# Kernel tuning notes

Measured on AMD Instinct MI355X. Metric: run time of the kernel, lower is better.

## Reference

```python
import jax, jax.numpy as jnp
import numpy as np

# Module config (matches init_kwargs)
STRIDE = (2, 2)
PAD = (1, 1)
OUT_PAD = (1, 1)
K = (3, 3)
MULTIPLIER = 2.0
CIN, COUT = 256, 256


def setup_inputs() -> dict:
    key = jax.random.key(0)
    k1, k2, k3 = jax.random.split(key, 3)
    B, H_in, W_in = 32, 64, 64
    x = jax.random.normal(k1, (B, CIN, H_in, W_in), dtype=jnp.float32)
    # kaiming-uniform-ish scale for weight, small uniform bias
    fan_in = CIN * K[0] * K[1]
    bound = 1.0 / np.sqrt(fan_in)
    weight = jax.random.uniform(k2, (CIN, COUT, K[0], K[1]), dtype=jnp.float32,
                                minval=-bound, maxval=bound)
    bias = jax.random.uniform(k3, (COUT,), dtype=jnp.float32, minval=-bound, maxval=bound)
    return {"x": x, "weight": weight, "bias": bias}


def _valid_mask(n_in, k, stride, pad, n_out):
    # mask[i, t] = 1.0 if 0 <= i*stride - pad + t < n_out
    i = jnp.arange(n_in)[:, None]
    t = jnp.arange(k)[None, :]
    o = i * stride - pad + t
    return ((o >= 0) & (o < n_out)).astype(jnp.float32)


def reference(x, weight, bias):
    B, Cin, H_in, W_in = x.shape
    Kh, Kw = weight.shape[2], weight.shape[3]
    H_out = (H_in - 1) * STRIDE[0] - 2 * PAD[0] + (Kh - 1) + OUT_PAD[0] + 1
    W_out = (W_in - 1) * STRIDE[1] - 2 * PAD[1] + (Kw - 1) + OUT_PAD[1] + 1

    mh = _valid_mask(H_in, Kh, STRIDE[0], PAD[0], H_out)  # [H_in, Kh]
    mw = _valid_mask(W_in, Kw, STRIDE[1], PAD[1], W_out)  # [W_in, Kw]

    # Stage 1: U[b,c,kh,kw] = sum_{h,w} x[b,c,h,w] * mh[h,kh] * mw[w,kw]
    U = jnp.einsum('bchw,hk,wl->bckl', x, mh, mw)
    # Stage 2: spatial sum per output channel
    S = jnp.einsum('bckl,cokl->bo', U, weight)
    spatial = H_out * W_out
    out = MULTIPLIER * (S / spatial + bias[None, :])
    return out.reshape(B, weight.shape[1], 1, 1)
```

## Files before the change

### kernel.cpp

```cpp
#include <hip/hip_runtime.h>

#define CIN   256
#define COUT  256
#define NB    32
#define HIN   64
#define WIN   64
#define SPATIAL_OUT 16384.0f
#define MULT  2.0f

__global__ __launch_bounds__(256) void reduce_x_kernel(
    const float* __restrict__ x, float* __restrict__ xs)
{
    const int bc = blockIdx.x;
    const float4* p = (const float4*)(x + (size_t)bc * (HIN * WIN));
    const int t = threadIdx.x;

    float s_all = 0.f, s_r0 = 0.f, s_c0 = 0.f, x00 = 0.f;
#pragma unroll
    for (int i = 0; i < 4; ++i) {
        const int idx = t + 256 * i;
        const float4 v = p[idx];
        s_all += v.x + v.y + v.z + v.w;
        if (idx < 16)        s_r0 += v.x + v.y + v.z + v.w;
        if ((idx & 15) == 0) s_c0 += v.x;
        if (idx == 0)        x00 = v.x;
    }

#pragma unroll
    for (int off = 32; off > 0; off >>= 1) {
        s_all += __shfl_down(s_all, off);
        s_r0  += __shfl_down(s_r0,  off);
        s_c0  += __shfl_down(s_c0,  off);
    }

    __shared__ float red[4][3];
    const int wave = t >> 6, lane = t & 63;
    if (lane == 0) { red[wave][0] = s_all; red[wave][1] = s_r0; red[wave][2] = s_c0; }
    __syncthreads();
    if (t == 0) {
        float a = 0.f, r = 0.f, c = 0.f;
#pragma unroll
        for (int w = 0; w < 4; ++w) { a += red[w][0]; r += red[w][1]; c += red[w][2]; }
        float4 o; o.x = a; o.y = r; o.z = c; o.w = x00;
        ((float4*)xs)[bc] = o;
    }
}

__global__ __launch_bounds__(256) void reduce_w_kernel(
    const float* __restrict__ w, float* __restrict__ ws)
{
    const int co = blockIdx.x * 256 + threadIdx.x;
    const float* p = w + (size_t)co * 9;
    const float w0 = p[0], w1 = p[1], w2 = p[2],
                w3 = p[3], w4 = p[4], w5 = p[5],
                w6 = p[6], w7 = p[7], w8 = p[8];
    const float wsum = w0 + w1 + w2 + w3 + w4 + w5 + w6 + w7 + w8;
    const float wr   = w0 + w1 + w2;
    const float wc   = w0 + w3 + w6;
    const int c = co >> 8, o = co & 255;
    ws[(c * 4 + 0) * 256 + o] = wsum;
    ws[(c * 4 + 1) * 256 + o] = wr;
    ws[(c * 4 + 2) * 256 + o] = wc;
    ws[(c * 4 + 3) * 256 + o] = w0;
}

__global__ __launch_bounds__(256) void finalize_kernel(
    const float* __restrict__ xs, const float* __restrict__ ws,
    const float* __restrict__ bias, float* __restrict__ out)
{
    const int b = blockIdx.x, o = threadIdx.x;
    __shared__ float4 sx[CIN];
    sx[o] = ((const float4*)xs)[b * CIN + o];
    __syncthreads();

    float acc = 0.f;
#pragma unroll 4
    for (int c = 0; c < CIN; ++c) {
        const float4 s = sx[c];
        const float wsum = ws[(c * 4 + 0) * 256 + o];
        const float wr   = ws[(c * 4 + 1) * 256 + o];
        const float wc   = ws[(c * 4 + 2) * 256 + o];
        const float w00  = ws[(c * 4 + 3) * 256 + o];
        acc += s.x * wsum - s.y * wr - s.z * wc + s.w * w00;
    }
    out[b * 256 + o] = MULT * (acc * (1.0f / SPATIAL_OUT) + bias[o]);
}

extern "C" void kernel_launch(void* const* d_in, const int* in_sizes, int n_in,
                              void* d_out, int out_size, void* d_ws, size_t ws_size,
                              hipStream_t stream)
{
    const float* x      = (const float*)d_in[0];
    const float* weight = (const float*)d_in[1];
    const float* bias   = (const float*)d_in[2];
    float* out = (float*)d_out;

    float* xs = (float*)d_ws;
    float* ws = xs + (size_t)NB * CIN * 4;

    reduce_x_kernel<<<NB * CIN, 256, 0, stream>>>(x, xs);
    reduce_w_kernel<<<CIN, 256, 0, stream>>>(weight, ws);
    finalize_kernel<<<NB, 256, 0, stream>>>(xs, ws, bias, out);
}
```

Measured before the change: 217.0 us.

## Merge x and weight stat kernels, pack weight stats as float4, split finalize

```diff
diff --git a/kernel.cpp b/kernel.cpp
--- a/kernel.cpp
+++ b/kernel.cpp
@@ -5,85 +5,89 @@
 #define NB    32
 #define HIN   64
 #define WIN   64
-#define SPATIAL_OUT 16384.0f
+#define INV_SPATIAL (1.0f / 16384.0f)
 #define MULT  2.0f
 
-__global__ __launch_bounds__(256) void reduce_x_kernel(
-    const float* __restrict__ x, float* __restrict__ xs)
+__global__ __launch_bounds__(256) void stats_kernel(
+    const float* __restrict__ x, const float* __restrict__ w,
+    float4* __restrict__ xs, float4* __restrict__ ws4)
 {
-    const int bc = blockIdx.x;
-    const float4* p = (const float4*)(x + (size_t)bc * (HIN * WIN));
-    const int t = threadIdx.x;
+    const int blk = blockIdx.x;
+    const int t   = threadIdx.x;
 
-    float s_all = 0.f, s_r0 = 0.f, s_c0 = 0.f, x00 = 0.f;
+    if (blk < NB * CIN) {
+        const float4* p = (const float4*)(x + (size_t)blk * (HIN * WIN));
+        float s_all = 0.f, s_r0 = 0.f, s_c0 = 0.f, x00 = 0.f;
 #pragma unroll
-    for (int i = 0; i < 4; ++i) {
-        const int idx = t + 256 * i;
-        const float4 v = p[idx];
-        s_all += v.x + v.y + v.z + v.w;
-        if (idx < 16)        s_r0 += v.x + v.y + v.z + v.w;
-        if ((idx & 15) == 0) s_c0 += v.x;
-        if (idx == 0)        x00 = v.x;
-    }
-
+        for (int i = 0; i < 4; ++i) {
+            const int idx = t + 256 * i;
+            const float4 v = p[idx];
+            s_all += v.x + v.y + v.z + v.w;
+            if (idx < 16)        s_r0 += v.x + v.y + v.z + v.w;
+            if ((idx & 15) == 0) s_c0 += v.x;
+            if (idx == 0)        x00 = v.x;
+        }
 #pragma unroll
-    for (int off = 32; off > 0; off >>= 1) {
-        s_all += __shfl_down(s_all, off);
-        s_r0  += __shfl_down(s_r0,  off);
-        s_c0  += __shfl_down(s_c0,  off);
-    }
-
-    __shared__ float red[4][3];
-    const int wave = t >> 6, lane = t & 63;
-    if (lane == 0) { red[wave][0] = s_all; red[wave][1] = s_r0; red[wave][2] = s_c0; }
-    __syncthreads();
-    if (t == 0) {
-        float a = 0.f, r = 0.f, c = 0.f;
+        for (int off = 32; off > 0; off >>= 1) {
+            s_all += __shfl_down(s_all, off);
+            s_r0  += __shfl_down(s_r0,  off);
+            s_c0  += __shfl_down(s_c0,  off);
+        }
+        __shared__ float red[4][3];
+        const int wave = t >> 6, lane = t & 63;
+        if (lane == 0) { red[wave][0] = s_all; red[wave][1] = s_r0; red[wave][2] = s_c0; }
+        __syncthreads();
+        if (t == 0) {
+            float a = 0.f, r = 0.f, c = 0.f;
 #pragma unroll
-        for (int w = 0; w < 4; ++w) { a += red[w][0]; r += red[w][1]; c += red[w][2]; }
-        float4 o; o.x = a; o.y = r; o.z = c; o.w = x00;
-        ((float4*)xs)[bc] = o;
+            for (int wv = 0; wv < 4; ++wv) { a += red[wv][0]; r += red[wv][1]; c += red[wv][2]; }
+            float4 o4; o4.x = a; o4.y = r; o4.z = c; o4.w = x00;
+            xs[blk] = o4;
+        }
+    } else {
+        const int c = blk - NB * CIN;
+        const float* p = w + ((size_t)c * COUT + t) * 9;
+        const float w0 = p[0], w1 = p[1], w2 = p[2],
+                    w3 = p[3], w4 = p[4], w5 = p[5],
+                    w6 = p[6], w7 = p[7], w8 = p[8];
+        float4 o4;
+        o4.x = w0 + w1 + w2 + w3 + w4 + w5 + w6 + w7 + w8;
+        o4.y = w0 + w1 + w2;
+        o4.z = w0 + w3 + w6;
+        o4.w = w0;
+        ws4[c * COUT + t] = o4;
     }
 }
 
-__global__ __launch_bounds__(256) void reduce_w_kernel(
-    const float* __restrict__ w, float* __restrict__ ws)
-{
-    const int co = blockIdx.x * 256 + threadIdx.x;
-    const float* p = w + (size_t)co * 9;
-    const float w0 = p[0], w1 = p[1], w2 = p[2],
-                w3 = p[3], w4 = p[4], w5 = p[5],
-                w6 = p[6], w7 = p[7], w8 = p[8];
-    const float wsum = w0 + w1 + w2 + w3 + w4 + w5 + w6 + w7 + w8;
-    const float wr   = w0 + w1 + w2;
-    const float wc   = w0 + w3 + w6;
-    const int c = co >> 8, o = co & 255;
-    ws[(c * 4 + 0) * 256 + o] = wsum;
-    ws[(c * 4 + 1) * 256 + o] = wr;
-    ws[(c * 4 + 2) * 256 + o] = wc;
-    ws[(c * 4 + 3) * 256 + o] = w0;
-}
-
-__global__ __launch_bounds__(256) void finalize_kernel(
-    const float* __restrict__ xs, const float* __restrict__ ws,
+__global__ __launch_bounds__(1024) void finalize_kernel(
+    const float4* __restrict__ xs, const float4* __restrict__ ws4,
     const float* __restrict__ bias, float* __restrict__ out)
 {
-    const int b = blockIdx.x, o = threadIdx.x;
+    const int b   = blockIdx.x;
+    const int t   = threadIdx.x;
+    const int o   = t & 255;
+    const int seg = t >> 8;
+
     __shared__ float4 sx[CIN];
-    sx[o] = ((const float4*)xs)[b * CIN + o];
+    __shared__ float  part[4][COUT];
+    if (t < CIN) sx[t] = xs[b * CIN + t];
     __syncthreads();
 
     float acc = 0.f;
-#pragma unroll 4
-    for (int c = 0; c < CIN; ++c) {
-        const float4 s = sx[c];
-        const float wsum = ws[(c * 4 + 0) * 256 + o];
-        const float wr   = ws[(c * 4 + 1) * 256 + o];
-        const float wc   = ws[(c * 4 + 2) * 256 + o];
-        const float w00  = ws[(c * 4 + 3) * 256 + o];
-        acc += s.x * wsum - s.y * wr - s.z * wc + s.w * w00;
+    const int c0 = seg * 64;
+#pragma unroll 8
+    for (int i = 0; i < 64; ++i) {
+        const int c = c0 + i;
+        const float4 s  = sx[c];
+        const float4 wv = ws4[c * COUT + o];
+        acc += s.x * wv.x - s.y * wv.y - s.z * wv.z + s.w * wv.w;
     }
-    out[b * 256 + o] = MULT * (acc * (1.0f / SPATIAL_OUT) + bias[o]);
+    part[seg][o] = acc;
+    __syncthreads();
+    if (t < COUT) {
+        const float a = part[0][t] + part[1][t] + part[2][t] + part[3][t];
+        out[b * COUT + t] = MULT * (a * INV_SPATIAL + bias[t]);
+    }
 }
 
 extern "C" void kernel_launch(void* const* d_in, const int* in_sizes, int n_in,
@@ -95,10 +99,9 @@
     const float* bias   = (const float*)d_in[2];
     float* out = (float*)d_out;
 
-    float* xs = (float*)d_ws;
-    float* ws = xs + (size_t)NB * CIN * 4;
+    float4* xs  = (float4*)d_ws;
+    float4* ws4 = xs + (size_t)NB * CIN;
 
-    reduce_x_kernel<<<NB * CIN, 256, 0, stream>>>(x, xs);
-    reduce_w_kernel<<<CIN, 256, 0, stream>>>(weight, ws);
-    finalize_kernel<<<NB, 256, 0, stream>>>(xs, ws, bias, out);
+    stats_kernel<<<NB * CIN + CIN, 256, 0, stream>>>(x, weight, xs, ws4);
+    finalize_kernel<<<NB, 1024, 0, stream>>>(xs, ws4, bias, out);
 }
```

New measurement: 200.8 us. -7.5%, faster.
